# Kernel optimization log

Measured on AMD Instinct MI355X. Metric: run time of the kernel, lower is better.

Reference implementation:

```python
import jax, jax.numpy as jnp
import numpy as np

B, P, N, E, H, D = 8, 1000, 1000, 128, 8, 16  # batch, pomo, nodes, embed, heads, qkv_dim
SQRT_E = float(np.sqrt(E))
CLIP = 10.0
INV_SQRT_D = 1.0 / float(np.sqrt(D))


def _heads(x):
    # [b, n, H*D] -> [b, H, n, D]
    b, n, _ = x.shape
    return x.reshape(b, n, H, D).transpose(0, 2, 1, 3)


def _mha(q, k, v, ninf_mask):
    # q: [b,H,P,D], k/v: [b,H,N,D], ninf_mask: [b,P,N]
    score = jnp.einsum('bhnd,bhsd->bhns', q, k) * INV_SQRT_D
    score = score + ninf_mask[:, None, :, :]
    w = jax.nn.softmax(score, axis=-1)
    out = jnp.einsum('bhns,bhsd->bhnd', w, v)
    return out.transpose(0, 2, 1, 3).reshape(q.shape[0], q.shape[2], H * D)


def setup_inputs() -> dict:
    key = jax.random.key(0)
    ks = jax.random.split(key, 16)
    s = 0.02
    return {
        'encoded_last_node': jax.random.normal(ks[0], (B, P, E), jnp.float32),
        'attr': jax.random.normal(ks[1], (B, P, 4), jnp.float32),
        'encoded_nodes': jax.random.normal(ks[2], (B, N, E), jnp.float32),
        'ninf_mask': jnp.zeros((B, P, N), jnp.float32),
        'Wq_shared': jax.random.normal(ks[3], (E + 4, H * D), jnp.float32) * s,
        'Wk_shared': jax.random.normal(ks[4], (E, H * D), jnp.float32) * s,
        'Wv_shared': jax.random.normal(ks[5], (E, H * D), jnp.float32) * s,
        'Wq_task': jax.random.normal(ks[6], (E + 4, H * D), jnp.float32) * s,
        'Wk_task': jax.random.normal(ks[7], (E, H * D), jnp.float32) * s,
        'Wv_task': jax.random.normal(ks[8], (E, H * D), jnp.float32) * s,
        'Wc_shared': jax.random.normal(ks[9], (H * D, E), jnp.float32) * s,
        'bc_shared': jnp.zeros((E,), jnp.float32),
        'Wc_task': jax.random.normal(ks[10], (H * D, E), jnp.float32) * s,
        'bc_task': jnp.zeros((E,), jnp.float32),
        'Wg': jax.random.normal(ks[11], (E + 4, E), jnp.float32) * s,
        'bg': jnp.zeros((E,), jnp.float32),
    }


def reference(encoded_last_node, attr, encoded_nodes, ninf_mask,
              Wq_shared, Wk_shared, Wv_shared, Wq_task, Wk_task, Wv_task,
              Wc_shared, bc_shared, Wc_task, bc_task, Wg, bg):
    # set_kv
    k_shared = _heads(encoded_nodes @ Wk_shared)
    v_shared = _heads(encoded_nodes @ Wv_shared)
    k_task = _heads(encoded_nodes @ Wk_task)
    v_task = _heads(encoded_nodes @ Wv_task)

    # decoder forward
    input_cat = jnp.concatenate([encoded_last_node, attr], axis=2)  # [B,P,E+4]
    q_shared = _heads(input_cat @ Wq_shared)
    q_task = _heads(input_cat @ Wq_task)

    out_shared = _mha(q_shared, k_shared, v_shared, ninf_mask) @ Wc_shared + bc_shared
    out_task = _mha(q_task, k_task, v_task, ninf_mask) @ Wc_task + bc_task

    gate = jax.nn.sigmoid(input_cat @ Wg + bg)
    gated_out = gate * out_shared + (1.0 - gate) * out_task  # [B,P,E]

    # pointer scores against single-head key (encoded_nodes)
    score = jnp.einsum('bpe,bne->bpn', gated_out, encoded_nodes) / SQRT_E
    score_clipped = CLIP * jnp.tanh(score)
    probs = jax.nn.softmax(score_clipped + ninf_mask, axis=2)
    return probs
```

## Files before the change

kernel.cpp:

```cpp
#include <hip/hip_runtime.h>
#include <math.h>

#define BB 8
#define PP 1000
#define NN 1000
#define EE 128
#define HH 8
#define DD 16

#define INV_SQRT_E 0.08838834764831845f
#define INV_SQRT_D 0.25f

typedef short short8_t __attribute__((ext_vector_type(8)));
typedef float f32x4    __attribute__((ext_vector_type(4)));
typedef float f32x16   __attribute__((ext_vector_type(16)));
typedef __bf16 bf16x4  __attribute__((ext_vector_type(4)));
typedef __bf16 bf16x8  __attribute__((ext_vector_type(8)));

__device__ __forceinline__ float sigmoid_fast(float x) {
    return 1.f / (1.f + __expf(-x));
}
__device__ __forceinline__ float tanh_fast(float x) {
    x = fminf(fmaxf(x, -15.f), 15.f);
    float e = __expf(2.f * x);
    return (e - 1.f) / (e + 1.f);
}

__device__ __forceinline__ f32x4 mfma16(short8_t a, short8_t b, f32x4 c) {
    return __builtin_amdgcn_mfma_f32_16x16x32_bf16(a, b, c, 0, 0, 0);
}
__device__ __forceinline__ f32x16 mfma32(short8_t a, short8_t b, f32x16 c) {
    return __builtin_amdgcn_mfma_f32_32x32x16_bf16(a, b, c, 0, 0, 0);
}

__device__ __forceinline__ float sum16(float x) {
    int v;
    v = __builtin_amdgcn_update_dpp(0, __builtin_bit_cast(int, x), 0xB1, 0xF, 0xF, true);
    x += __builtin_bit_cast(float, v);
    v = __builtin_amdgcn_update_dpp(0, __builtin_bit_cast(int, x), 0x4E, 0xF, 0xF, true);
    x += __builtin_bit_cast(float, v);
    v = __builtin_amdgcn_update_dpp(0, __builtin_bit_cast(int, x), 0x141, 0xF, 0xF, true);
    x += __builtin_bit_cast(float, v);
    v = __builtin_amdgcn_update_dpp(0, __builtin_bit_cast(int, x), 0x140, 0xF, 0xF, true);
    x += __builtin_bit_cast(float, v);
    return x;
}

__global__ __launch_bounds__(256) void prep_kernel(
    const float* __restrict__ mask, const float* __restrict__ nodes,
    const float* __restrict__ eln,  const float* __restrict__ attr,
    const float* __restrict__ Wk_s, const float* __restrict__ Wv_s,
    const float* __restrict__ Wk_t, const float* __restrict__ Wv_t,
    const float* __restrict__ Wq_s, const float* __restrict__ Wq_t,
    const float* __restrict__ Wg,   const float* __restrict__ Wc_s,
    const float* __restrict__ Wc_t,
    __bf16* __restrict__ emaskb, __bf16* __restrict__ nodesb,
    __bf16* __restrict__ inb, __bf16* __restrict__ Wtb)
{
    const int bx = blockIdx.x;
    __shared__ float tile[32][129];
    if (bx < 7813) {
        int i = (bx * 256 + threadIdx.x) * 4;
        if (i < 8000000) {
            float4 v = *(const float4*)&mask[i];
            bf16x4 pk = { (__bf16)__expf(v.x), (__bf16)__expf(v.y),
                          (__bf16)__expf(v.z), (__bf16)__expf(v.w) };
            *(bf16x4*)&emaskb[i] = pk;
        }
    } else if (bx < 8813) {
        int i = ((bx - 7813) * 256 + threadIdx.x) * 4;
        float4 v = *(const float4*)&nodes[i];
        bf16x4 pk = { (__bf16)v.x, (__bf16)v.y, (__bf16)v.z, (__bf16)v.w };
        *(bf16x4*)&nodesb[i] = pk;
    } else if (bx < 9438) {
        int t = (bx - 8813) * 256 + threadIdx.x;
        int row = t / 20, seg = t - row * 20;
        bf16x8 o = {};
        if (seg < 16) {
            const float* p = &eln[(size_t)row * 128 + seg * 8];
            float4 a = *(const float4*)p, b = *(const float4*)(p + 4);
            o = bf16x8{ (__bf16)a.x, (__bf16)a.y, (__bf16)a.z, (__bf16)a.w,
                        (__bf16)b.x, (__bf16)b.y, (__bf16)b.z, (__bf16)b.w };
        } else if (seg == 16) {
            float4 a = *(const float4*)&attr[(size_t)row * 4];
            o = bf16x8{ (__bf16)a.x, (__bf16)a.y, (__bf16)a.z, (__bf16)a.w,
                        (__bf16)0.f, (__bf16)0.f, (__bf16)0.f, (__bf16)0.f };
        }
        *(bf16x8*)&inb[(size_t)row * 160 + seg * 8] = o;
    } else {
        int idx = bx - 9438;
        int m = idx / 5, kt = idx - m * 5;
        const float* srcs[9] = {Wk_s, Wv_s, Wk_t, Wv_t, Wq_s, Wq_t, Wg, Wc_s, Wc_t};
        const int   srcKs[9] = {128, 128, 128, 128, 132, 132, 132, 128, 128};
        const int   kpads[9] = {128, 128, 128, 128, 160, 160, 160, 128, 128};
        const size_t offs[9] = {0, 16384, 32768, 49152, 65536, 86016, 106496, 126976, 143360};
        const int kp = kpads[m];
        if (kt * 32 >= kp) return;
        const float* src = srcs[m];
        const int sK = srcKs[m];
        const size_t off = offs[m];
        const int tid = threadIdx.x;
        for (int j = tid; j < 32 * 128; j += 256) {
            int kk = j >> 7, n = j & 127;
            int k = kt * 32 + kk;
            tile[kk][n] = (k < sK) ? src[(size_t)k * 128 + n] : 0.f;
        }
        __syncthreads();
        for (int j = tid; j < 32 * 128; j += 256) {
            int n = j >> 5, kk = j & 31;
            Wtb[off + (size_t)n * kp + kt * 32 + kk] = (__bf16)tile[kk][n];
        }
    }
}

template<int NC>
__device__ __forceinline__ void proj_body(
    const __bf16* __restrict__ A, const __bf16* __restrict__ W,
    f32x4 acc[8], int r0, int quad, int lq)
{
    const int K = NC * 32;
    short8_t aF[NC];
    #pragma unroll
    for (int c = 0; c < NC; ++c)
        aF[c] = *(const short8_t*)&A[(size_t)(r0 + lq) * K + c * 32 + quad * 8];
    #pragma unroll
    for (int nt = 0; nt < 8; ++nt) {
        acc[nt] = f32x4{0.f, 0.f, 0.f, 0.f};
        #pragma unroll
        for (int c = 0; c < NC; ++c) {
            short8_t bF = *(const short8_t*)&W[(size_t)(nt * 16 + lq) * K + c * 32 + quad * 8];
            acc[nt] = mfma16(aF[c], bF, acc[nt]);
        }
    }
}

__global__ __launch_bounds__(256) void proj_mfma_kernel(
    const __bf16* __restrict__ nodesb, const __bf16* __restrict__ inb,
    const __bf16* __restrict__ Wtb,
    __bf16* __restrict__ kb_s, __bf16* __restrict__ vt_s,
    __bf16* __restrict__ kb_t, __bf16* __restrict__ vt_t,
    __bf16* __restrict__ qb_s, __bf16* __restrict__ qb_t)
{
    const int wsel = blockIdx.y;
    const int wave = threadIdx.x >> 6, lane = threadIdx.x & 63;
    const int quad = lane >> 4, lq = lane & 15;
    const int r0 = blockIdx.x * 64 + wave * 16;

    f32x4 acc[8];
    if (wsel < 4) {
        proj_body<4>(nodesb, Wtb + (size_t)wsel * 16384, acc, r0, quad, lq);
    } else {
        proj_body<5>(inb, Wtb + 65536 + (size_t)(wsel - 4) * 20480, acc, r0, quad, lq);
    }

    if (wsel == 0 || wsel == 2) {
        __bf16* O = (wsel == 0) ? kb_s : kb_t;
        #pragma unroll
        for (int r = 0; r < 4; ++r) {
            int m = r0 + quad * 4 + r;
            int b = m / 1000, n = m - b * 1000;
            #pragma unroll
            for (int nt = 0; nt < 8; ++nt)
                O[(((size_t)(b * 8 + nt) * 1000 + n) << 4) + lq] = (__bf16)acc[nt][r];
        }
    } else if (wsel == 4 || wsel == 5) {
        __bf16* O = (wsel == 4) ? qb_s : qb_t;
        #pragma unroll
        for (int r = 0; r < 4; ++r) {
            int m = r0 + quad * 4 + r;
            int b = m / 1000, n = m - b * 1000;
            #pragma unroll
            for (int nt = 0; nt < 8; ++nt)
                O[(((size_t)(b * 8 + nt) * 1000 + n) << 4) + lq] =
                    (__bf16)(acc[nt][r] * INV_SQRT_D);
        }
    } else {
        __bf16* O = (wsel == 1) ? vt_s : vt_t;
        #pragma unroll
        for (int r = 0; r < 4; ++r) {
            int m = r0 + quad * 4 + r;
            int b = m / 1000, n = m - b * 1000;
            int rr = n & 31;
            int pos = (n & ~31) + ((rr < 16) ? (rr << 1) : (((rr - 16) << 1) | 1));
            #pragma unroll
            for (int nt = 0; nt < 8; ++nt)
                O[(((size_t)(b * 8 + nt) * 16 + lq) << 10) + pos] = (__bf16)acc[nt][r];
        }
    }
}

__global__ __launch_bounds__(256) void attn_mfma_kernel(
    const __bf16* __restrict__ qb_s, const __bf16* __restrict__ qb_t,
    const __bf16* __restrict__ kb_s, const __bf16* __restrict__ kb_t,
    const __bf16* __restrict__ vt_s, const __bf16* __restrict__ vt_t,
    const __bf16* __restrict__ emaskb,
    __bf16* __restrict__ att_s, __bf16* __restrict__ att_t)
{
    const int b    = blockIdx.z;
    const int wave = threadIdx.x >> 6;
    const int combo = blockIdx.y * 4 + wave;
    const int br = combo & 1;
    const int h  = combo >> 1;
    const __bf16* Q  = br ? qb_t : qb_s;
    const __bf16* K  = br ? kb_t : kb_s;
    const __bf16* Vt = br ? vt_t : vt_s;
    __bf16* O        = br ? att_t : att_s;
    const int lane = threadIdx.x & 63;
    const int quad = lane >> 4, lq = lane & 15;
    const int col  = lane & 31;
    const int half = lane >> 5;
    const int bh = b * HH + h;
    const int p0 = blockIdx.x * 32;

    __shared__ __align__(16) __bf16 S[4][32][36];

    int pq = p0 + col; if (pq > 999) pq = 999;
    short8_t qA = *(const short8_t*)&Q[(((size_t)bh * 1000 + pq) << 4) + half * 8];

    short8_t onesB = { (short)0x3F80, (short)0x3F80, (short)0x3F80, (short)0x3F80,
                       (short)0x3F80, (short)0x3F80, (short)0x3F80, (short)0x3F80 };

    f32x4 o[2] = { {0.f,0.f,0.f,0.f}, {0.f,0.f,0.f,0.f} };
    f32x4 l[2] = { {0.f,0.f,0.f,0.f}, {0.f,0.f,0.f,0.f} };

    const __bf16* mrow[8];
    #pragma unroll
    for (int j = 0; j < 8; ++j) {
        int row = p0 + ((2 * j) & 3) + 8 * (j >> 1) + 4 * half;
        if (row > 998) row = 998;
        mrow[j] = emaskb + ((size_t)b * 1000 + row) * 1000 + col;
    }

    short8_t kBc = *(const short8_t*)&K[(((size_t)bh * 1000 + col) << 4) + half * 8];
    short8_t vBc = *(const short8_t*)&Vt[(((size_t)bh * 16 + lq) << 10) + quad * 8];

    for (int n0 = 0; n0 < 992; n0 += 32) {
        int nk = n0 + 32 + col; if (nk > 999) nk = 999;
        short8_t kBn = *(const short8_t*)&K[(((size_t)bh * 1000 + nk) << 4) + half * 8];
        short8_t vBn = *(const short8_t*)&Vt[(((size_t)bh * 16 + lq) << 10) + n0 + 32 + quad * 8];

        float mk[16];
        #pragma unroll
        for (int j = 0; j < 8; ++j) {
            mk[2 * j]     = (float)mrow[j][0];
            mk[2 * j + 1] = (float)mrow[j][1000];
            mrow[j] += 32;
        }

        f32x16 s = mfma32(qA, kBc, f32x16{});

        __threadfence_block();
        #pragma unroll
        for (int reg = 0; reg < 16; ++reg) {
            float e = __expf(s[reg]) * mk[reg];
            S[wave][(reg & 3) + 8 * (reg >> 2) + 4 * half][col] = (__bf16)e;
        }
        __threadfence_block();

        #pragma unroll
        for (int t = 0; t < 2; ++t) {
            uint2 L = *(const uint2*)&S[wave][t * 16 + lq][quad * 4];
            uint2 H = *(const uint2*)&S[wave][t * 16 + lq][16 + quad * 4];
            unsigned u0 = __builtin_amdgcn_perm(H.x, L.x, 0x05040100u);
            unsigned u1 = __builtin_amdgcn_perm(H.x, L.x, 0x07060302u);
            unsigned u2 = __builtin_amdgcn_perm(H.y, L.y, 0x05040100u);
            unsigned u3 = __builtin_amdgcn_perm(H.y, L.y, 0x07060302u);
            uint4 u4 = make_uint4(u0, u1, u2, u3);
            short8_t aP = __builtin_bit_cast(short8_t, u4);
            o[t] = mfma16(aP, vBc, o[t]);
            l[t] = mfma16(aP, onesB, l[t]);
        }
        kBc = kBn; vBc = vBn;
    }

    {
        f32x16 s = mfma32(qA, kBc, f32x16{});
        __threadfence_block();
        #pragma unroll
        for (int reg = 0; reg < 16; ++reg) {
            int j = reg >> 1;
            float mkv = (col < 8) ? (float)((reg & 1) ? mrow[j][1000] : mrow[j][0]) : 0.f;
            float e = __expf(s[reg]) * mkv;
            S[wave][(reg & 3) + 8 * (reg >> 2) + 4 * half][col] = (__bf16)e;
        }
        __threadfence_block();
        #pragma unroll
        for (int t = 0; t < 2; ++t) {
            uint2 L = *(const uint2*)&S[wave][t * 16 + lq][quad * 4];
            uint2 H = *(const uint2*)&S[wave][t * 16 + lq][16 + quad * 4];
            unsigned u0 = __builtin_amdgcn_perm(H.x, L.x, 0x05040100u);
            unsigned u1 = __builtin_amdgcn_perm(H.x, L.x, 0x07060302u);
            unsigned u2 = __builtin_amdgcn_perm(H.y, L.y, 0x05040100u);
            unsigned u3 = __builtin_amdgcn_perm(H.y, L.y, 0x07060302u);
            uint4 u4 = make_uint4(u0, u1, u2, u3);
            short8_t aP = __builtin_bit_cast(short8_t, u4);
            o[t] = mfma16(aP, vBc, o[t]);
            l[t] = mfma16(aP, onesB, l[t]);
        }
    }

    #pragma unroll
    for (int t = 0; t < 2; ++t)
        #pragma unroll
        for (int r = 0; r < 4; ++r) {
            int p = p0 + t * 16 + quad * 4 + r;
            if (p < 1000)
                O[((size_t)b * 1000 + p) * 128 + h * 16 + lq] = (__bf16)(o[t][r] / l[t][r]);
        }
}

__global__ __launch_bounds__(128) void combine_mfma_kernel(
    const __bf16* __restrict__ att_s, const __bf16* __restrict__ att_t,
    const __bf16* __restrict__ inb, const __bf16* __restrict__ Wtb,
    const float* __restrict__ bc_s, const float* __restrict__ bc_t,
    const float* __restrict__ bg, __bf16* __restrict__ gatedb)
{
    const int wave = threadIdx.x >> 6, lane = threadIdx.x & 63;
    const int quad = lane >> 4, lq = lane & 15;
    const int r0 = blockIdx.x * 32 + wave * 16;
    const __bf16* Wgp = Wtb + 106496;
    const __bf16* Ws  = Wtb + 126976;
    const __bf16* Wt  = Wtb + 143360;

    short8_t aS[4], aT[4], aG[5];
    #pragma unroll
    for (int c = 0; c < 4; ++c) {
        aS[c] = *(const short8_t*)&att_s[(size_t)(r0 + lq) * 128 + c * 32 + quad * 8];
        aT[c] = *(const short8_t*)&att_t[(size_t)(r0 + lq) * 128 + c * 32 + quad * 8];
    }
    #pragma unroll
    for (int c = 0; c < 5; ++c)
        aG[c] = *(const short8_t*)&inb[(size_t)(r0 + lq) * 160 + c * 32 + quad * 8];

    #pragma unroll
    for (int nt = 0; nt < 8; ++nt) {
        f32x4 accS = {0.f,0.f,0.f,0.f}, accT = accS, accG = accS;
        #pragma unroll
        for (int c = 0; c < 4; ++c) {
            short8_t bS = *(const short8_t*)&Ws[(size_t)(nt * 16 + lq) * 128 + c * 32 + quad * 8];
            short8_t bT = *(const short8_t*)&Wt[(size_t)(nt * 16 + lq) * 128 + c * 32 + quad * 8];
            accS = mfma16(aS[c], bS, accS);
            accT = mfma16(aT[c], bT, accT);
        }
        #pragma unroll
        for (int c = 0; c < 5; ++c) {
            short8_t bG = *(const short8_t*)&Wgp[(size_t)(nt * 16 + lq) * 160 + c * 32 + quad * 8];
            accG = mfma16(aG[c], bG, accG);
        }
        int f = nt * 16 + lq;
        float b1 = bc_s[f], b2 = bc_t[f], b3 = bg[f];
        #pragma unroll
        for (int r = 0; r < 4; ++r) {
            int m = r0 + quad * 4 + r;
            float g = sigmoid_fast(accG[r] + b3);
            float val = g * (accS[r] + b1) + (1.f - g) * (accT[r] + b2);
            gatedb[(size_t)m * 128 + f] = (__bf16)val;
        }
    }
}

__global__ __launch_bounds__(256) void pointer_softmax_kernel(
    const __bf16* __restrict__ gb, const __bf16* __restrict__ nb,
    const __bf16* __restrict__ emaskb, float* __restrict__ out)
{
    const int b    = blockIdx.y;
    const int p0   = blockIdx.x * 16;
    const int wave = threadIdx.x >> 6;
    const int lane = threadIdx.x & 63;
    const int quad = lane >> 4, lq = lane & 15;

    __shared__ float Spart[4][16];

    short8_t aF[4];
    {
        int pp = p0 + lq; if (pp > 999) pp = 999;
        const __bf16* arow = gb + (((size_t)b * 1000 + pp) << 7) + quad * 8;
        #pragma unroll
        for (int kc = 0; kc < 4; ++kc) aF[kc] = *(const short8_t*)&arow[kc * 32];
    }

    float ev[16][4];
    float psum[4] = {0.f, 0.f, 0.f, 0.f};

    #pragma unroll
    for (int i = 0; i < 16; ++i) {
        const int nt = i * 4 + wave;
        const int nn = nt * 16 + lq;
        const bool nv = nn < 1000;
        int nc = nv ? nn : 999;
        const __bf16* brow = nb + (((size_t)b * 1000 + nc) << 7) + quad * 8;
        f32x4 acc = {0.f, 0.f, 0.f, 0.f};
        #pragma unroll
        for (int kc = 0; kc < 4; ++kc) {
            short8_t bF = *(const short8_t*)&brow[kc * 32];
            acc = mfma16(aF[kc], bF, acc);
        }
        #pragma unroll
        for (int r = 0; r < 4; ++r) {
            int p = p0 + quad * 4 + r;
            bool v = nv && (p < 1000);
            size_t midx = v ? ((size_t)b * 1000 + p) * 1000 + nn : 0;
            float mk = (float)emaskb[midx];
            float sc = 10.f * tanh_fast(acc[r] * INV_SQRT_E);
            float ee = v ? __expf(sc) * mk : 0.f;
            ev[i][r] = ee;
            psum[r] += ee;
        }
    }

    #pragma unroll
    for (int r = 0; r < 4; ++r) psum[r] = sum16(psum[r]);
    if (lq == 0) {
        #pragma unroll
        for (int r = 0; r < 4; ++r) Spart[wave][quad * 4 + r] = psum[r];
    }
    __syncthreads();
    float inv[4];
    #pragma unroll
    for (int r = 0; r < 4; ++r) {
        int row = quad * 4 + r;
        float s = Spart[0][row] + Spart[1][row] + Spart[2][row] + Spart[3][row];
        inv[r] = 1.f / s;
    }

    #pragma unroll
    for (int i = 0; i < 16; ++i) {
        const int nt = i * 4 + wave;
        const int nn = nt * 16 + lq;
        if (nn < 1000) {
            #pragma unroll
            for (int r = 0; r < 4; ++r) {
                int p = p0 + quad * 4 + r;
                if (p < 1000)
                    out[((size_t)b * 1000 + p) * 1000 + nn] = ev[i][r] * inv[r];
            }
        }
    }
}

extern "C" void kernel_launch(void* const* d_in, const int* in_sizes, int n_in,
                              void* d_out, int out_size, void* d_ws, size_t ws_size,
                              hipStream_t stream)
{
    const float* eln   = (const float*)d_in[0];
    const float* attr  = (const float*)d_in[1];
    const float* nodes = (const float*)d_in[2];
    const float* mask  = (const float*)d_in[3];
    const float* Wq_s  = (const float*)d_in[4];
    const float* Wk_s  = (const float*)d_in[5];
    const float* Wv_s  = (const float*)d_in[6];
    const float* Wq_t  = (const float*)d_in[7];
    const float* Wk_t  = (const float*)d_in[8];
    const float* Wv_t  = (const float*)d_in[9];
    const float* Wc_s  = (const float*)d_in[10];
    const float* bc_s  = (const float*)d_in[11];
    const float* Wc_t  = (const float*)d_in[12];
    const float* bc_t  = (const float*)d_in[13];
    const float* Wg    = (const float*)d_in[14];
    const float* bg    = (const float*)d_in[15];
    float* out = (float*)d_out;

    char* w = (char*)d_ws;
    const size_t KB_SZ = (size_t)64 * 1000 * 16 * 2;
    const size_t VT_SZ = (size_t)64 * 16 * 1024 * 2;
    const size_t H_SZ  = (size_t)8000 * 128 * 2;
    const size_t IN_SZ = (size_t)8000 * 160 * 2;
    const size_t EM_SZ = (size_t)8000 * 1000 * 2;
    __bf16* kb_s  = (__bf16*)w;           w += KB_SZ;
    __bf16* kb_t  = (__bf16*)w;           w += KB_SZ;
    __bf16* qb_s  = (__bf16*)w;           w += KB_SZ;
    __bf16* qb_t  = (__bf16*)w;           w += KB_SZ;
    __bf16* vt_s  = (__bf16*)w;           w += VT_SZ;
    __bf16* vt_t  = (__bf16*)w;           w += VT_SZ;
    __bf16* att_s = (__bf16*)w;           w += H_SZ;
    __bf16* att_t = (__bf16*)w;           w += H_SZ;
    __bf16* gatedb = (__bf16*)w;          w += H_SZ;
    __bf16* nodesb = (__bf16*)w;          w += H_SZ;
    __bf16* inb    = (__bf16*)w;          w += IN_SZ;
    __bf16* emaskb = (__bf16*)w;          w += EM_SZ;
    __bf16* Wtb    = (__bf16*)w;          w += 320000;

    hipMemsetAsync(vt_s, 0, 2 * VT_SZ, stream);

    prep_kernel<<<dim3(9483), 256, 0, stream>>>(
        mask, nodes, eln, attr, Wk_s, Wv_s, Wk_t, Wv_t, Wq_s, Wq_t, Wg,
        Wc_s, Wc_t, emaskb, nodesb, inb, Wtb);
    proj_mfma_kernel<<<dim3(125, 6), 256, 0, stream>>>(
        nodesb, inb, Wtb, kb_s, vt_s, kb_t, vt_t, qb_s, qb_t);
    attn_mfma_kernel<<<dim3(32, 4, 8), 256, 0, stream>>>(
        qb_s, qb_t, kb_s, kb_t, vt_s, vt_t, emaskb, att_s, att_t);
    combine_mfma_kernel<<<dim3(250), 128, 0, stream>>>(
        att_s, att_t, inb, Wtb, bc_s, bc_t, bg, gatedb);
    pointer_softmax_kernel<<<dim3(63, 8), 256, 0, stream>>>(
        gatedb, nodesb, emaskb, out);
}
```

Measured before the change: 232.5 us.

## Transpose score MFMA, store mask in log2 domain, use exp2 in attention

The QK MFMA operand order is swapped so that each lane holds contiguous key positions for one query. This lets the mask be read as contiguous bf16x4 vectors and lets the P tile be written and read from LDS as straight vectors, removing the perm-based repacking. The mask is now stored as log2e-scaled additive values, and the query is prescaled by log2e/sqrt(D), so exp2 can be applied to score plus mask instead of expf times a precomputed exp(mask). This also changes bf16 rounding: the additive mask is stored in bf16, and masked -inf still maps to zero through exp2.

```diff
diff --git a/kernel.cpp b/kernel.cpp
--- a/kernel.cpp
+++ b/kernel.cpp
@@ -9,7 +9,8 @@
 #define DD 16
 
 #define INV_SQRT_E 0.08838834764831845f
-#define INV_SQRT_D 0.25f
+#define LOG2E      1.4426950408889634f
+#define QSCALE     0.3606737602222409f
 
 typedef short short8_t __attribute__((ext_vector_type(8)));
 typedef float f32x4    __attribute__((ext_vector_type(4)));
@@ -63,8 +64,8 @@
         int i = (bx * 256 + threadIdx.x) * 4;
         if (i < 8000000) {
             float4 v = *(const float4*)&mask[i];
-            bf16x4 pk = { (__bf16)__expf(v.x), (__bf16)__expf(v.y),
-                          (__bf16)__expf(v.z), (__bf16)__expf(v.w) };
+            bf16x4 pk = { (__bf16)(v.x * LOG2E), (__bf16)(v.y * LOG2E),
+                          (__bf16)(v.z * LOG2E), (__bf16)(v.w * LOG2E) };
             *(bf16x4*)&emaskb[i] = pk;
         }
     } else if (bx < 8813) {
@@ -172,7 +173,7 @@
             #pragma unroll
             for (int nt = 0; nt < 8; ++nt)
                 O[(((size_t)(b * 8 + nt) * 1000 + n) << 4) + lq] =
-                    (__bf16)(acc[nt][r] * INV_SQRT_D);
+                    (__bf16)(acc[nt][r] * QSCALE);
         }
     } else {
         __bf16* O = (wsel == 1) ? vt_s : vt_t;
@@ -212,10 +213,12 @@
     const int bh = b * HH + h;
     const int p0 = blockIdx.x * 32;
 
-    __shared__ __align__(16) __bf16 S[4][32][36];
+    __shared__ __align__(16) __bf16 S[4][32][40];
 
     int pq = p0 + col; if (pq > 999) pq = 999;
-    short8_t qA = *(const short8_t*)&Q[(((size_t)bh * 1000 + pq) << 4) + half * 8];
+    short8_t qB = *(const short8_t*)&Q[(((size_t)bh * 1000 + pq) << 4) + half * 8];
+
+    const __bf16* mp = emaskb + ((size_t)b * 1000 + pq) * 1000 + 4 * half;
 
     short8_t onesB = { (short)0x3F80, (short)0x3F80, (short)0x3F80, (short)0x3F80,
                        (short)0x3F80, (short)0x3F80, (short)0x3F80, (short)0x3F80 };
@@ -223,77 +226,60 @@
     f32x4 o[2] = { {0.f,0.f,0.f,0.f}, {0.f,0.f,0.f,0.f} };
     f32x4 l[2] = { {0.f,0.f,0.f,0.f}, {0.f,0.f,0.f,0.f} };
 
-    const __bf16* mrow[8];
-    #pragma unroll
-    for (int j = 0; j < 8; ++j) {
-        int row = p0 + ((2 * j) & 3) + 8 * (j >> 1) + 4 * half;
-        if (row > 998) row = 998;
-        mrow[j] = emaskb + ((size_t)b * 1000 + row) * 1000 + col;
-    }
-
-    short8_t kBc = *(const short8_t*)&K[(((size_t)bh * 1000 + col) << 4) + half * 8];
+    short8_t kAc = *(const short8_t*)&K[(((size_t)bh * 1000 + col) << 4) + half * 8];
     short8_t vBc = *(const short8_t*)&Vt[(((size_t)bh * 16 + lq) << 10) + quad * 8];
 
     for (int n0 = 0; n0 < 992; n0 += 32) {
         int nk = n0 + 32 + col; if (nk > 999) nk = 999;
-        short8_t kBn = *(const short8_t*)&K[(((size_t)bh * 1000 + nk) << 4) + half * 8];
+        short8_t kAn = *(const short8_t*)&K[(((size_t)bh * 1000 + nk) << 4) + half * 8];
         short8_t vBn = *(const short8_t*)&Vt[(((size_t)bh * 16 + lq) << 10) + n0 + 32 + quad * 8];
 
-        float mk[16];
-        #pragma unroll
-        for (int j = 0; j < 8; ++j) {
-            mk[2 * j]     = (float)mrow[j][0];
-            mk[2 * j + 1] = (float)mrow[j][1000];
-            mrow[j] += 32;
-        }
-
-        f32x16 s = mfma32(qA, kBc, f32x16{});
-
-        __threadfence_block();
-        #pragma unroll
-        for (int reg = 0; reg < 16; ++reg) {
-            float e = __expf(s[reg]) * mk[reg];
-            S[wave][(reg & 3) + 8 * (reg >> 2) + 4 * half][col] = (__bf16)e;
-        }
-        __threadfence_block();
+        bf16x4 m2[4];
+        #pragma unroll
+        for (int g = 0; g < 4; ++g)
+            m2[g] = *(const bf16x4*)&mp[n0 + 8 * g];
+
+        f32x16 s = mfma32(kAc, qB, f32x16{});
+
+        __builtin_amdgcn_sched_barrier(0x7F);
+        #pragma unroll
+        for (int g = 0; g < 4; ++g) {
+            bf16x4 pk;
+            #pragma unroll
+            for (int j = 0; j < 4; ++j)
+                pk[j] = (__bf16)__builtin_amdgcn_exp2f(s[4 * g + j] + (float)m2[g][j]);
+            *(bf16x4*)&S[wave][col][8 * g + 4 * half] = pk;
+        }
+        __builtin_amdgcn_sched_barrier(0x7F);
 
         #pragma unroll
         for (int t = 0; t < 2; ++t) {
-            uint2 L = *(const uint2*)&S[wave][t * 16 + lq][quad * 4];
-            uint2 H = *(const uint2*)&S[wave][t * 16 + lq][16 + quad * 4];
-            unsigned u0 = __builtin_amdgcn_perm(H.x, L.x, 0x05040100u);
-            unsigned u1 = __builtin_amdgcn_perm(H.x, L.x, 0x07060302u);
-            unsigned u2 = __builtin_amdgcn_perm(H.y, L.y, 0x05040100u);
-            unsigned u3 = __builtin_amdgcn_perm(H.y, L.y, 0x07060302u);
-            uint4 u4 = make_uint4(u0, u1, u2, u3);
-            short8_t aP = __builtin_bit_cast(short8_t, u4);
+            short8_t aP = *(const short8_t*)&S[wave][t * 16 + lq][quad * 8];
             o[t] = mfma16(aP, vBc, o[t]);
             l[t] = mfma16(aP, onesB, l[t]);
         }
-        kBc = kBn; vBc = vBn;
+        kAc = kAn; vBc = vBn;
     }
 
     {
-        f32x16 s = mfma32(qA, kBc, f32x16{});
-        __threadfence_block();
-        #pragma unroll
-        for (int reg = 0; reg < 16; ++reg) {
-            int j = reg >> 1;
-            float mkv = (col < 8) ? (float)((reg & 1) ? mrow[j][1000] : mrow[j][0]) : 0.f;
-            float e = __expf(s[reg]) * mkv;
-            S[wave][(reg & 3) + 8 * (reg >> 2) + 4 * half][col] = (__bf16)e;
-        }
-        __threadfence_block();
+        bf16x4 m2t = *(const bf16x4*)&mp[992];
+        f32x16 s = mfma32(kAc, qB, f32x16{});
+
+        __builtin_amdgcn_sched_barrier(0x7F);
+        bf16x4 pk0;
+        #pragma unroll
+        for (int j = 0; j < 4; ++j)
+            pk0[j] = (__bf16)__builtin_amdgcn_exp2f(s[j] + (float)m2t[j]);
+        *(bf16x4*)&S[wave][col][4 * half] = pk0;
+        bf16x4 z = {};
+        #pragma unroll
+        for (int g = 1; g < 4; ++g)
+            *(bf16x4*)&S[wave][col][8 * g + 4 * half] = z;
+        __builtin_amdgcn_sched_barrier(0x7F);
+
         #pragma unroll
         for (int t = 0; t < 2; ++t) {
-            uint2 L = *(const uint2*)&S[wave][t * 16 + lq][quad * 4];
-            uint2 H = *(const uint2*)&S[wave][t * 16 + lq][16 + quad * 4];
-            unsigned u0 = __builtin_amdgcn_perm(H.x, L.x, 0x05040100u);
-            unsigned u1 = __builtin_amdgcn_perm(H.x, L.x, 0x07060302u);
-            unsigned u2 = __builtin_amdgcn_perm(H.y, L.y, 0x05040100u);
-            unsigned u3 = __builtin_amdgcn_perm(H.y, L.y, 0x07060302u);
-            uint4 u4 = make_uint4(u0, u1, u2, u3);
-            short8_t aP = __builtin_bit_cast(short8_t, u4);
+            short8_t aP = *(const short8_t*)&S[wave][t * 16 + lq][quad * 8];
             o[t] = mfma16(aP, vBc, o[t]);
             l[t] = mfma16(aP, onesB, l[t]);
         }
@@ -400,9 +386,9 @@
             int p = p0 + quad * 4 + r;
             bool v = nv && (p < 1000);
             size_t midx = v ? ((size_t)b * 1000 + p) * 1000 + nn : 0;
-            float mk = (float)emaskb[midx];
+            float m2 = (float)emaskb[midx];
             float sc = 10.f * tanh_fast(acc[r] * INV_SQRT_E);
-            float ee = v ? __expf(sc) * mk : 0.f;
+            float ee = v ? __builtin_amdgcn_exp2f(sc * LOG2E + m2) : 0.f;
             ev[i][r] = ee;
             psum[r] += ee;
         }
```

After: 233.5 us. No clear change (+0.4%).
